# Optimization experiments

Hardware: AMD Instinct MI355X
Metric: run time of the kernel (lower is better)

## Reference

```python
import jax, jax.numpy as jnp
import numpy as np

B, S, D = 16, 2048, 768
NORM = 1.0 / float(np.sqrt(D))


def setup_inputs() -> dict:
    key = jax.random.key(0)
    k1, k2, k3, k4, k5 = jax.random.split(key, 5)
    b_in = jax.random.normal(k1, (B, S, D), dtype=jnp.float32)
    mask = jax.random.randint(k2, (B, S), 0, 2, dtype=jnp.int64)
    # row 0 must be unmasked: the module returns attention[:, 0, :], and a fully
    # masked query row softmaxes all -inf -> NaN (same quirk as the torch source).
    mask = mask.at[:, 0].set(1)
    Wq = jax.random.normal(k3, (D, D), dtype=jnp.float32) * 0.02
    Wk = jax.random.normal(k4, (D, D), dtype=jnp.float32) * 0.02
    Wv = jax.random.normal(k5, (D, D), dtype=jnp.float32) * 0.02
    return {"b_in": b_in, "mask": mask, "Wq": Wq, "Wk": Wk, "Wv": Wv}


def reference(b_in, mask, Wq, Wk, Wv):
    # nn.Linear(bias=False): y = x @ W.T  (W is [out, in])
    q = jnp.einsum("bsd,ed->bse", b_in, Wq)
    k = jnp.einsum("bsd,ed->bse", b_in, Wk)
    v = jnp.einsum("bsd,ed->bse", b_in, Wv)
    # full [B, S, S] score matrix, as in the original bmm
    scores = jnp.einsum("bqd,bkd->bqk", q, k) * NORM
    # mask.unsqueeze(2): [B, S, 1] broadcasts over the KEY axis -> masks whole query rows
    scores = jnp.where(mask[:, :, None] == 0, -jnp.inf, scores)
    attn = jax.nn.softmax(scores, axis=-1)
    out = jnp.einsum("bqk,bkd->bqd", attn, v)
    return out[:, 0, :]
```

## Files before the change

kernel.cpp:

```cpp
#include <hip/hip_runtime.h>
#include <math.h>

#define BB 16
#define SS 2048
#define DD 768

#define NORM_SCALE 0.036084391824351615f

#define ECH 24
#define EPC (DD / ECH)

#define RPC 16
#define NCH (SS / RPC)

__global__ void rowdot_kernel(const float* __restrict__ src, size_t src_stride,
                              const float* __restrict__ W,
                              float* __restrict__ dst, float scale,
                              float* __restrict__ zero_buf) {
    int wid  = blockIdx.x * 4 + (threadIdx.x >> 6);
    int lane = threadIdx.x & 63;
    int b = wid / DD;
    int e = wid % DD;
    const float4* xr = (const float4*)(src + (size_t)b * src_stride);
    const float4* wr = (const float4*)(W + (size_t)e * DD);
    float acc = 0.f;
#pragma unroll
    for (int k = 0; k < 3; ++k) {
        float4 xv = xr[lane + k * 64];
        float4 wv = wr[lane + k * 64];
        acc += xv.x * wv.x + xv.y * wv.y + xv.z * wv.z + xv.w * wv.w;
    }
#pragma unroll
    for (int off = 32; off > 0; off >>= 1) acc += __shfl_down(acc, off);
    if (lane == 0) dst[wid] = acc * scale;
    if (zero_buf != nullptr && lane == 1) zero_buf[wid] = 0.f;
}

__global__ void kq_split_kernel(const float* __restrict__ q0,
                                const float* __restrict__ Wk,
                                float* __restrict__ kqs) {
    __shared__ float qs[EPC];
    int echunk = blockIdx.x;
    int b      = blockIdx.y;
    int t      = threadIdx.x;
    if (t < EPC) qs[t] = q0[b * DD + echunk * EPC + t];
    __syncthreads();
    const float4* Wk4 = (const float4*)(Wk + (size_t)(echunk * EPC) * DD);
    float4 acc = {0.f, 0.f, 0.f, 0.f};
#pragma unroll 4
    for (int e = 0; e < EPC; ++e) {
        float q = qs[e];
        float4 w = Wk4[e * (DD / 4) + t];
        acc.x += q * w.x;
        acc.y += q * w.y;
        acc.z += q * w.z;
        acc.w += q * w.w;
    }
    float* dst = kqs + b * DD + t * 4;
    atomicAdd(dst + 0, acc.x);
    atomicAdd(dst + 1, acc.y);
    atomicAdd(dst + 2, acc.z);
    atomicAdd(dst + 3, acc.w);
}

__global__ void flash_kernel(const float* __restrict__ x,
                             const float* __restrict__ kqs,
                             float* __restrict__ m_part,
                             float* __restrict__ l_part,
                             float* __restrict__ o_part) {
    __shared__ float xs[RPC * DD];
    __shared__ float sc[RPC];
    __shared__ float p[RPC];
    __shared__ float mbc[1];
    int chunk = blockIdx.x;
    int b     = blockIdx.y;
    int tid   = threadIdx.x;
    int wave  = tid >> 6, lane = tid & 63;
    int s0    = chunk * RPC;

    const float4* kr = (const float4*)(kqs + b * DD);
    float4 kf0 = kr[lane];
    float4 kf1 = kr[lane + 64];
    float4 kf2 = kr[lane + 128];

#pragma unroll
    for (int j = 0; j < 4; ++j) {
        int r = wave * 4 + j;
        const float4* xr = (const float4*)(x + ((size_t)b * SS + s0 + r) * DD);
        float4 x0 = xr[lane];
        float4 x1 = xr[lane + 64];
        float4 x2 = xr[lane + 128];
        float4* xsr = (float4*)(xs + r * DD);
        xsr[lane]       = x0;
        xsr[lane + 64]  = x1;
        xsr[lane + 128] = x2;
        float acc = x0.x * kf0.x + x0.y * kf0.y + x0.z * kf0.z + x0.w * kf0.w
                  + x1.x * kf1.x + x1.y * kf1.y + x1.z * kf1.z + x1.w * kf1.w
                  + x2.x * kf2.x + x2.y * kf2.y + x2.z * kf2.z + x2.w * kf2.w;
#pragma unroll
        for (int off = 32; off > 0; off >>= 1) acc += __shfl_down(acc, off);
        if (lane == 0) sc[r] = acc;
    }
    __syncthreads();

    if (tid == 0) {
        float m = sc[0];
#pragma unroll
        for (int r = 1; r < RPC; ++r) m = fmaxf(m, sc[r]);
        mbc[0] = m;
    }
    __syncthreads();
    if (tid < RPC) p[tid] = expf(sc[tid] - mbc[0]);
    __syncthreads();

    float a0 = 0.f, a1 = 0.f, a2 = 0.f;
#pragma unroll
    for (int r = 0; r < RPC; ++r) {
        float pr = p[r];
        a0 += pr * xs[r * DD + tid];
        a1 += pr * xs[r * DD + tid + 256];
        a2 += pr * xs[r * DD + tid + 512];
    }
    int pidx = b * NCH + chunk;
    float* op = o_part + (size_t)pidx * DD;
    op[tid]       = a0;
    op[tid + 256] = a1;
    op[tid + 512] = a2;
    if (tid == 0) {
        float l = 0.f;
#pragma unroll
        for (int r = 0; r < RPC; ++r) l += p[r];
        m_part[pidx] = mbc[0];
        l_part[pidx] = l;
    }
}

__global__ void combine_kernel(const float* __restrict__ m_part,
                               const float* __restrict__ l_part,
                               const float* __restrict__ o_part,
                               float* __restrict__ c) {
    __shared__ float w[NCH];
    __shared__ float bc[2];
    int b = blockIdx.x;
    int tid = threadIdx.x;

    if (tid < NCH) w[tid] = m_part[b * NCH + tid];
    __syncthreads();
    if (tid == 0) {
        float M = w[0];
        for (int i = 1; i < NCH; ++i) M = fmaxf(M, w[i]);
        bc[0] = M;
    }
    __syncthreads();
    float M = bc[0];
    if (tid < NCH) w[tid] = expf(w[tid] - M);
    __syncthreads();
    if (tid == 0) {
        float l = 0.f;
        for (int i = 0; i < NCH; ++i) l += w[i] * l_part[b * NCH + i];
        bc[1] = 1.f / l;
    }
    __syncthreads();
    float inv = bc[1];

    float a0 = 0.f, a1 = 0.f, a2 = 0.f;
    const float* op = o_part + (size_t)b * NCH * DD;
#pragma unroll 4
    for (int cc = 0; cc < NCH; ++cc) {
        float wc = w[cc];
        const float* o = op + (size_t)cc * DD;
        a0 += wc * o[tid];
        a1 += wc * o[tid + 256];
        a2 += wc * o[tid + 512];
    }
    c[b * DD + tid]       = a0 * inv;
    c[b * DD + tid + 256] = a1 * inv;
    c[b * DD + tid + 512] = a2 * inv;
}

extern "C" void kernel_launch(void* const* d_in, const int* in_sizes, int n_in,
                              void* d_out, int out_size, void* d_ws, size_t ws_size,
                              hipStream_t stream) {
    const float* b_in = (const float*)d_in[0];
    const float* Wq = (const float*)d_in[2];
    const float* Wk = (const float*)d_in[3];
    const float* Wv = (const float*)d_in[4];
    float* out = (float*)d_out;

    float* ws     = (float*)d_ws;
    float* q0     = ws;
    float* kqs    = q0 + BB * DD;
    float* m_part = kqs + BB * DD;
    float* l_part = m_part + BB * NCH;
    float* o_part = l_part + BB * NCH;
    float* c      = o_part + (size_t)BB * NCH * DD;

    rowdot_kernel<<<BB * DD / 4, 256, 0, stream>>>(b_in, (size_t)SS * DD, Wq,
                                                   q0, NORM_SCALE, kqs);
    kq_split_kernel<<<dim3(ECH, BB), 192, 0, stream>>>(q0, Wk, kqs);
    flash_kernel<<<dim3(NCH, BB), 256, 0, stream>>>(b_in, kqs,
                                                    m_part, l_part, o_part);
    combine_kernel<<<BB, 256, 0, stream>>>(m_part, l_part, o_part, c);
    rowdot_kernel<<<BB * DD / 4, 256, 0, stream>>>(c, (size_t)DD, Wv, out,
                                                   1.f, nullptr);
}
```

Measured before the change: 191.3 us.

## Load flash tiles directly into LDS and split combine across column segments

The flash kernel now stages its 16x768 input tile straight from global memory into LDS with global_load_lds, so the data no longer passes through registers before the shared-memory store. The score dot products then read back from LDS after a barrier. Separately, the combine kernel is launched with three column segments per batch, giving 48 blocks instead of 16 and more parallelism for the partial-output reduction. The direct-to-LDS path adds a block-wide barrier before any compute, depends on the builtin's lane-addressing layout being right, and each combine block repeats the max/sum setup.

```diff
diff --git a/kernel.cpp b/kernel.cpp
--- a/kernel.cpp
+++ b/kernel.cpp
@@ -63,11 +63,12 @@
     atomicAdd(dst + 3, acc.w);
 }
 
-__global__ void flash_kernel(const float* __restrict__ x,
-                             const float* __restrict__ kqs,
-                             float* __restrict__ m_part,
-                             float* __restrict__ l_part,
-                             float* __restrict__ o_part) {
+__global__ void __launch_bounds__(256) flash_kernel(
+        const float* __restrict__ x,
+        const float* __restrict__ kqs,
+        float* __restrict__ m_part,
+        float* __restrict__ l_part,
+        float* __restrict__ o_part) {
     __shared__ float xs[RPC * DD];
     __shared__ float sc[RPC];
     __shared__ float p[RPC];
@@ -78,22 +79,30 @@
     int wave  = tid >> 6, lane = tid & 63;
     int s0    = chunk * RPC;
 
+    const float* xg = x + ((size_t)b * SS + s0 + wave * 4) * DD;
+    float*       xl = xs + wave * 4 * DD;
+#pragma unroll
+    for (int k = 0; k < 12; ++k) {
+        __builtin_amdgcn_global_load_lds(
+            (const __attribute__((address_space(1))) unsigned int*)(xg + k * 256 + lane * 4),
+            (__attribute__((address_space(3))) unsigned int*)(xl + k * 256),
+            16, 0, 0);
+    }
+
     const float4* kr = (const float4*)(kqs + b * DD);
     float4 kf0 = kr[lane];
     float4 kf1 = kr[lane + 64];
     float4 kf2 = kr[lane + 128];
 
+    __syncthreads();
+
 #pragma unroll
     for (int j = 0; j < 4; ++j) {
         int r = wave * 4 + j;
-        const float4* xr = (const float4*)(x + ((size_t)b * SS + s0 + r) * DD);
-        float4 x0 = xr[lane];
-        float4 x1 = xr[lane + 64];
-        float4 x2 = xr[lane + 128];
-        float4* xsr = (float4*)(xs + r * DD);
-        xsr[lane]       = x0;
-        xsr[lane + 64]  = x1;
-        xsr[lane + 128] = x2;
+        const float4* xsr = (const float4*)(xs + r * DD);
+        float4 x0 = xsr[lane];
+        float4 x1 = xsr[lane + 64];
+        float4 x2 = xsr[lane + 128];
         float acc = x0.x * kf0.x + x0.y * kf0.y + x0.z * kf0.z + x0.w * kf0.w
                   + x1.x * kf1.x + x1.y * kf1.y + x1.z * kf1.z + x1.w * kf1.w
                   + x2.x * kf2.x + x2.y * kf2.y + x2.z * kf2.z + x2.w * kf2.w;
@@ -141,7 +150,8 @@
                                float* __restrict__ c) {
     __shared__ float w[NCH];
     __shared__ float bc[2];
-    int b = blockIdx.x;
+    int b   = blockIdx.x;
+    int seg = blockIdx.y;
     int tid = threadIdx.x;
 
     if (tid < NCH) w[tid] = m_part[b * NCH + tid];
@@ -163,19 +173,12 @@
     __syncthreads();
     float inv = bc[1];
 
-    float a0 = 0.f, a1 = 0.f, a2 = 0.f;
-    const float* op = o_part + (size_t)b * NCH * DD;
-#pragma unroll 4
-    for (int cc = 0; cc < NCH; ++cc) {
-        float wc = w[cc];
-        const float* o = op + (size_t)cc * DD;
-        a0 += wc * o[tid];
-        a1 += wc * o[tid + 256];
-        a2 += wc * o[tid + 512];
-    }
-    c[b * DD + tid]       = a0 * inv;
-    c[b * DD + tid + 256] = a1 * inv;
-    c[b * DD + tid + 512] = a2 * inv;
+    int col = seg * 256 + tid;
+    const float* op = o_part + (size_t)b * NCH * DD + col;
+    float a = 0.f;
+#pragma unroll 8
+    for (int cc = 0; cc < NCH; ++cc) a += w[cc] * op[(size_t)cc * DD];
+    c[b * DD + col] = a * inv;
 }
 
 extern "C" void kernel_launch(void* const* d_in, const int* in_sizes, int n_in,
@@ -200,7 +203,7 @@
     kq_split_kernel<<<dim3(ECH, BB), 192, 0, stream>>>(q0, Wk, kqs);
     flash_kernel<<<dim3(NCH, BB), 256, 0, stream>>>(b_in, kqs,
                                                     m_part, l_part, o_part);
-    combine_kernel<<<BB, 256, 0, stream>>>(m_part, l_part, o_part, c);
+    combine_kernel<<<dim3(BB, 3), 256, 0, stream>>>(m_part, l_part, o_part, c);
     rowdot_kernel<<<BB * DD / 4, 256, 0, stream>>>(c, (size_t)DD, Wv, out,
                                                    1.f, nullptr);
 }
```

Result: faster. 185.5 us (-3.0%).
